# Kernel tuning notes

Hardware: AMD Instinct MI355X
Metric: run time of the kernel (lower is better)

## Reference

```python
import jax, jax.numpy as jnp
import numpy as np

N, E, F, H, G = 50000, 800000, 64, 64, 100

def setup_inputs() -> dict:
    key = jax.random.key(0)
    ks = jax.random.split(key, 12)
    x = jax.random.normal(ks[0], (N, F), dtype=jnp.float32)
    edge_index = jax.random.randint(ks[1], (2, E), 0, N, dtype=jnp.int64)
    batch = jnp.sort(jax.random.randint(ks[2], (N,), 0, G, dtype=jnp.int64))
    s1 = 1.0 / np.sqrt(F); s2 = 1.0 / np.sqrt(H)
    W1 = jax.random.normal(ks[3], (2, F, H), dtype=jnp.float32) * s1
    b1 = jnp.zeros((H,), dtype=jnp.float32)
    W2 = jax.random.normal(ks[4], (2, H, H), dtype=jnp.float32) * s2
    b2 = jnp.zeros((H,), dtype=jnp.float32)
    gamma = jnp.ones((H,), dtype=jnp.float32)
    beta = jnp.zeros((H,), dtype=jnp.float32)
    linW = jax.random.normal(ks[5], (H, 1), dtype=jnp.float32) * s2
    linb = jnp.zeros((1,), dtype=jnp.float32)
    return {"x": x, "edge_index": edge_index, "batch": batch, "W1": W1, "b1": b1,
            "W2": W2, "b2": b2, "gamma": gamma, "beta": beta, "linW": linW, "linb": linb}

def _edge_norm(row, col, n):
    # get_laplacian(sym) + lambda_max=2: Lhat off-diag weight = -d_i^{-1/2} d_j^{-1/2}, diag = 0
    deg = jax.ops.segment_sum(jnp.ones(row.shape[0], jnp.float32), row, num_segments=n)
    dis = jnp.where(deg > 0, deg ** -0.5, 0.0)
    return -dis[row] * dis[col]

def _cheb(x, row, col, w, W, b):
    # K=2: out = T0(Lhat)x @ W0 + T1(Lhat)x @ W1 + b, T1 = Lhat x via scatter-add
    Tx1 = jax.ops.segment_sum(w[:, None] * x[row], col, num_segments=x.shape[0])
    return x @ W[0] + Tx1 @ W[1] + b

def reference(x, edge_index, batch, W1, b1, W2, b2, gamma, beta, linW, linb):
    row, col = edge_index[0], edge_index[1]
    n = x.shape[0]
    w = _edge_norm(row, col, n)
    h = _cheb(x, row, col, w, W1, b1)
    # BatchNorm1d (training-mode batch stats, eps=1e-5)
    mu = jnp.mean(h, axis=0)
    var = jnp.var(h, axis=0)
    h = (h - mu) * jax.lax.rsqrt(var + 1e-5) * gamma + beta
    # LeakyReLU (default slope 0.01)
    h = jnp.where(h >= 0, h, 0.01 * h)
    h = _cheb(h, row, col, w, W2, b2)
    # global_mean_pool over graph ids
    sums = jax.ops.segment_sum(h, batch, num_segments=G)
    cnts = jax.ops.segment_sum(jnp.ones(n, jnp.float32), batch, num_segments=G)
    pooled = sums / jnp.maximum(cnts, 1.0)[:, None]
    # dropout: identity (eval)
    return pooled @ linW + linb
```

## Files before the change

### kernel.cpp

```cpp
#include <hip/hip_runtime.h>

#define HDIM 64
#define BH 64
#define HNODES 25600
#define HBINS 12800
#define SBINS 12544
#define GR 32


__device__ __forceinline__ int lbound(const int* __restrict__ b, int n, int v) {
    int lo = 0, hi = n;
    while (lo < hi) { int m = (lo + hi) >> 1; if (b[m] < v) lo = m + 1; else hi = m; }
    return lo;
}


__global__ __launch_bounds__(256) void k_histP(const int* __restrict__ row,
                                               const int* __restrict__ col,
                                               unsigned short* __restrict__ cntP,
                                               unsigned short* __restrict__ degP,
                                               int E, int N, int slice) {
    __shared__ unsigned hbin[HBINS];
    int blk   = blockIdx.x;
    int phase = blockIdx.y & 1;
    int isRow = blockIdx.y >> 1;
    const int* keys = isRow ? row : col;
    unsigned short* outP = isRow ? degP : cntP;
    int lo = phase * HNODES;
    int spanN = min(HNODES, N - lo);
    int binsU = (spanN + 1) >> 1;
    for (int i = threadIdx.x; i < binsU; i += 256) hbin[i] = 0;
    __syncthreads();
    int e0 = blk * slice, e1 = min(e0 + slice, E);
    for (int e = e0 + threadIdx.x; e < e1; e += 256) {
        int c = keys[e] - lo;
        if ((unsigned)c < (unsigned)spanN)
            atomicAdd(&hbin[c >> 1], 1u << ((c & 1) << 4));
    }
    __syncthreads();
    unsigned* outU = (unsigned*)(outP + (size_t)blk * N + lo);
    for (int i = threadIdx.x; i < binsU; i += 256) outU[i] = hbin[i];
}

__global__ void k_prefA(unsigned short* __restrict__ cntP,
                        const unsigned short* __restrict__ degP,
                        int* __restrict__ cnt, float* __restrict__ dis, int N) {
    int i = blockIdx.x * blockDim.x + threadIdx.x;
    if (i >= N) return;
    int run = 0;
    #pragma unroll 8
    for (int b = 0; b < BH; ++b) {
        int v = cntP[(size_t)b * N + i];
        cntP[(size_t)b * N + i] = (unsigned short)run;
        run += v;
    }
    cnt[i] = run;
    int d = 0;
    #pragma unroll 8
    for (int b = 0; b < BH; ++b) d += degP[(size_t)b * N + i];
    dis[i] = d > 0 ? rsqrtf((float)d) : 0.0f;
}

__global__ __launch_bounds__(1024) void k_scan1(const int* __restrict__ cnt,
                                                int* __restrict__ start,
                                                int* __restrict__ bsum, int n) {
    __shared__ int wsum[16];
    int i = blockIdx.x * 1024 + threadIdx.x;
    int lane = threadIdx.x & 63, w = threadIdx.x >> 6;
    int v = (i < n) ? cnt[i] : 0;
    int incl = v;
    #pragma unroll
    for (int off = 1; off < 64; off <<= 1) {
        int u = __shfl_up(incl, off, 64);
        if (lane >= off) incl += u;
    }
    if (lane == 63) wsum[w] = incl;
    __syncthreads();
    if (w == 0) {
        int s = (lane < 16) ? wsum[lane] : 0;
        int si = s;
        #pragma unroll
        for (int off = 1; off < 16; off <<= 1) {
            int u = __shfl_up(si, off, 64);
            if (lane >= off) si += u;
        }
        if (lane < 16) wsum[lane] = si - s;
    }
    __syncthreads();
    int excl = incl - v + wsum[w];
    if (i < n) start[i] = excl;
    if (threadIdx.x == 1023) bsum[blockIdx.x] = excl + v;
}

__global__ void k_scan2(int* __restrict__ bsum, int nb) {
    int lane = threadIdx.x;
    if (lane >= 64) return;
    int v = (lane < nb) ? bsum[lane] : 0;
    int incl = v;
    #pragma unroll
    for (int off = 1; off < 64; off <<= 1) {
        int u = __shfl_up(incl, off, 64);
        if (lane >= off) incl += u;
    }
    if (lane < nb) bsum[lane] = incl - v;
}

__global__ void k_scan3(int* __restrict__ start, const int* __restrict__ bsum, int n) {
    int i = blockIdx.x * blockDim.x + threadIdx.x;
    if (i < n) start[i] += bsum[i >> 10];
}

__global__ __launch_bounds__(256) void k_sortfill(const int* __restrict__ row,
                                                  const int* __restrict__ col,
                                                  const unsigned short* __restrict__ cntP,
                                                  const int* __restrict__ start,
                                                  int* __restrict__ er,
                                                  int E, int N, int slice) {
    __shared__ int cur[SBINS];
    int blk = blockIdx.x;
    int lo = blockIdx.y * SBINS;
    int span = min(SBINS, N - lo);
    for (int i = threadIdx.x; i < span; i += 256)
        cur[i] = start[lo + i] + (int)cntP[(size_t)blk * N + lo + i];
    __syncthreads();
    int e0 = blk * slice, e1 = min(e0 + slice, E);
    for (int e = e0 + threadIdx.x; e < e1; e += 256) {
        int c = col[e] - lo;
        int rv = row[e];
        if ((unsigned)c < (unsigned)span) {
            int pos = atomicAdd(&cur[c], 1);
            er[pos] = rv;
        }
    }
}


__global__ __launch_bounds__(256) void k_gather1(const int* __restrict__ er,
                                                 const int* __restrict__ start,
                                                 const int* __restrict__ cnt,
                                                 const float* __restrict__ dis,
                                                 const float* __restrict__ x,
                                                 float* __restrict__ Tx, int n) {
    int i = blockIdx.x * 4 + (threadIdx.x >> 6);
    if (i >= n) return;
    int lane = threadIdx.x & 63;
    int q = lane >> 4;
    int s4 = (lane & 15) * 4;
    int s = start[i], nd = cnt[i];
    float di = dis[i];
    float4 acc = make_float4(0.f, 0.f, 0.f, 0.f);
    int k = q;
    for (; k + 4 < nd; k += 8) {
        int r0 = er[s + k], r1 = er[s + k + 4];
        float w0 = -dis[r0] * di, w1 = -dis[r1] * di;
        float4 v0 = *reinterpret_cast<const float4*>(&x[(size_t)r0 * HDIM + s4]);
        float4 v1 = *reinterpret_cast<const float4*>(&x[(size_t)r1 * HDIM + s4]);
        acc.x = fmaf(w0, v0.x, acc.x); acc.y = fmaf(w0, v0.y, acc.y);
        acc.z = fmaf(w0, v0.z, acc.z); acc.w = fmaf(w0, v0.w, acc.w);
        acc.x = fmaf(w1, v1.x, acc.x); acc.y = fmaf(w1, v1.y, acc.y);
        acc.z = fmaf(w1, v1.z, acc.z); acc.w = fmaf(w1, v1.w, acc.w);
    }
    if (k < nd) {
        int r0 = er[s + k];
        float w0 = -dis[r0] * di;
        float4 v0 = *reinterpret_cast<const float4*>(&x[(size_t)r0 * HDIM + s4]);
        acc.x = fmaf(w0, v0.x, acc.x); acc.y = fmaf(w0, v0.y, acc.y);
        acc.z = fmaf(w0, v0.z, acc.z); acc.w = fmaf(w0, v0.w, acc.w);
    }
    #pragma unroll
    for (int off = 16; off <= 32; off <<= 1) {
        acc.x += __shfl_xor(acc.x, off, 64);
        acc.y += __shfl_xor(acc.y, off, 64);
        acc.z += __shfl_xor(acc.z, off, 64);
        acc.w += __shfl_xor(acc.w, off, 64);
    }
    if (q == 0) *reinterpret_cast<float4*>(&Tx[(size_t)i * HDIM + s4]) = acc;
}

__global__ __launch_bounds__(256) void k_gemm1(const float* __restrict__ x,
                                               float* __restrict__ TxH,
                                               const float* __restrict__ W1,
                                               const float* __restrict__ b1,
                                               float* __restrict__ stats, int n) {
    __shared__ float xs[GR][HDIM];
    __shared__ float ts[GR][HDIM];
    int tid = threadIdx.x;
    int j = tid & 63, w = tid >> 6;

    float4 w0r[16], w1r[16];
    #pragma unroll
    for (int k4 = 0; k4 < 16; ++k4) {
        w0r[k4].x = W1[(k4 * 4 + 0) * HDIM + j];
        w0r[k4].y = W1[(k4 * 4 + 1) * HDIM + j];
        w0r[k4].z = W1[(k4 * 4 + 2) * HDIM + j];
        w0r[k4].w = W1[(k4 * 4 + 3) * HDIM + j];
        w1r[k4].x = W1[4096 + (k4 * 4 + 0) * HDIM + j];
        w1r[k4].y = W1[4096 + (k4 * 4 + 1) * HDIM + j];
        w1r[k4].z = W1[4096 + (k4 * 4 + 2) * HDIM + j];
        w1r[k4].w = W1[4096 + (k4 * 4 + 3) * HDIM + j];
    }
    float bj = b1[j];
    float sacc = 0.f, ssacc = 0.f;

    for (int base = blockIdx.x * GR; base < n; base += gridDim.x * GR) {
        __syncthreads();
        for (int v = tid; v < GR * HDIM / 4; v += 256) {
            int r = base + (v >> 4);
            if (r < n) {
                int c = (v & 15) * 4;
                ((float4*)xs)[v] = *(const float4*)&x[(size_t)r * HDIM + c];
                ((float4*)ts)[v] = *(const float4*)&TxH[(size_t)r * HDIM + c];
            }
        }
        __syncthreads();
        #pragma unroll
        for (int m = 0; m < 8; ++m) {
            int lr = w * 8 + m;
            int r = base + lr;
            if (r < n) {
                const float4* xr = (const float4*)xs[lr];
                const float4* tr = (const float4*)ts[lr];
                float acc = bj;
                #pragma unroll
                for (int k4 = 0; k4 < 16; ++k4) {
                    float4 xv = xr[k4], tv = tr[k4];
                    acc = fmaf(xv.x, w0r[k4].x, acc);
                    acc = fmaf(xv.y, w0r[k4].y, acc);
                    acc = fmaf(xv.z, w0r[k4].z, acc);
                    acc = fmaf(xv.w, w0r[k4].w, acc);
                    acc = fmaf(tv.x, w1r[k4].x, acc);
                    acc = fmaf(tv.y, w1r[k4].y, acc);
                    acc = fmaf(tv.z, w1r[k4].z, acc);
                    acc = fmaf(tv.w, w1r[k4].w, acc);
                }
                TxH[(size_t)r * HDIM + j] = acc;
                sacc += acc;
                ssacc = fmaf(acc, acc, ssacc);
            }
        }
    }
    __syncthreads();
    xs[w][j] = sacc;
    ts[w][j] = ssacc;
    __syncthreads();
    if (w == 0) {
        float s  = xs[0][j] + xs[1][j] + xs[2][j] + xs[3][j];
        float ss = ts[0][j] + ts[1][j] + ts[2][j] + ts[3][j];
        atomicAdd(&stats[j], s);
        atomicAdd(&stats[64 + j], ss);
    }
}

__global__ void k_prep(const float* __restrict__ stats,
                       const float* __restrict__ gamma, const float* __restrict__ beta,
                       const float* __restrict__ W2, const float* __restrict__ b2,
                       const float* __restrict__ linW, const float* __restrict__ linb,
                       float* __restrict__ scale, float* __restrict__ shift,
                       float* __restrict__ u0, float* __restrict__ u1,
                       float* __restrict__ c0, int n) {
    int k = threadIdx.x;
    if (k >= HDIM) return;
    float inv_n = 1.0f / (float)n;
    float mu  = stats[k] * inv_n;
    float var = stats[64 + k] * inv_n - mu * mu;
    float rs  = rsqrtf(var + 1e-5f);
    float sc  = rs * gamma[k];
    scale[k] = sc;
    shift[k] = beta[k] - mu * sc;
    float a0 = 0.f, a1 = 0.f;
    #pragma unroll 8
    for (int j = 0; j < HDIM; ++j) {
        float lw = linW[j];
        a0 = fmaf(W2[k * HDIM + j], lw, a0);
        a1 = fmaf(W2[HDIM * HDIM + k * HDIM + j], lw, a1);
    }
    u0[k] = a0;
    u1[k] = a1;
    if (k == 0) {
        float c = linb[0];
        for (int j = 0; j < HDIM; ++j) c = fmaf(b2[j], linW[j], c);
        c0[0] = c;
    }
}

__global__ __launch_bounds__(256) void k_node(const float* __restrict__ h,
                                              const float* __restrict__ scale,
                                              const float* __restrict__ shift,
                                              const float* __restrict__ u0,
                                              const float* __restrict__ u1,
                                              float* __restrict__ a, float* __restrict__ t,
                                              int n) {
    int i = blockIdx.x * 4 + (threadIdx.x >> 6);
    if (i >= n) return;
    int j = threadIdx.x & 63;
    float v = fmaf(h[(size_t)i * HDIM + j], scale[j], shift[j]);
    v = v >= 0.f ? v : 0.01f * v;
    float p0 = v * u0[j];
    float p1 = v * u1[j];
    #pragma unroll
    for (int off = 32; off > 0; off >>= 1) {
        p0 += __shfl_xor(p0, off, 64);
        p1 += __shfl_xor(p1, off, 64);
    }
    if (j == 0) { a[i] = p0; t[i] = p1; }
}

__global__ void k_gather2(const int* __restrict__ er, const int* __restrict__ start,
                          const int* __restrict__ cnt, const float* __restrict__ dis,
                          const float* __restrict__ t, const float* __restrict__ a,
                          float* __restrict__ s2, int n) {
    int i = blockIdx.x * blockDim.x + threadIdx.x;
    if (i >= n) return;
    int s = start[i], nd = cnt[i];
    float di = dis[i];
    float acc = a[i];
    int k = 0;
    for (; k + 1 < nd; k += 2) {
        int r0 = er[s + k], r1 = er[s + k + 1];
        float v0 = -dis[r0] * di * t[r0];
        float v1 = -dis[r1] * di * t[r1];
        acc += v0 + v1;
    }
    if (k < nd) {
        int r0 = er[s + k];
        acc = fmaf(-dis[r0] * di, t[r0], acc);
    }
    s2[i] = acc;
}

__global__ __launch_bounds__(256) void k_pool2(const float* __restrict__ s2,
                                               const int* __restrict__ batch,
                                               const float* __restrict__ c0,
                                               const float* __restrict__ linb,
                                               float* __restrict__ out, int n) {
    int g = blockIdx.x;
    int lo = lbound(batch, n, g);
    int hi = lbound(batch, n, g + 1);
    float s = 0.f;
    for (int i = lo + threadIdx.x; i < hi; i += 256) s += s2[i];
    __shared__ float red[256];
    red[threadIdx.x] = s;
    __syncthreads();
    for (int off = 128; off > 0; off >>= 1) {
        if (threadIdx.x < off) red[threadIdx.x] += red[threadIdx.x + off];
        __syncthreads();
    }
    if (threadIdx.x == 0) {
        int cntg = hi - lo;
        out[g] = cntg > 0 ? red[0] / (float)cntg + c0[0] : linb[0];
    }
}


extern "C" void kernel_launch(void* const* d_in, const int* in_sizes, int n_in,
                              void* d_out, int out_size, void* d_ws, size_t ws_size,
                              hipStream_t stream) {
    const float* x     = (const float*)d_in[0];
    const int*   eidx  = (const int*)d_in[1];
    const int*   batch = (const int*)d_in[2];
    const float* W1    = (const float*)d_in[3];
    const float* b1    = (const float*)d_in[4];
    const float* W2    = (const float*)d_in[5];
    const float* b2    = (const float*)d_in[6];
    const float* gamma = (const float*)d_in[7];
    const float* beta  = (const float*)d_in[8];
    const float* linW  = (const float*)d_in[9];
    const float* linb  = (const float*)d_in[10];
    float* out = (float*)d_out;

    const int N = in_sizes[0] / HDIM;
    const int E = in_sizes[1] / 2;
    const int G = out_size;
    const int NB = (N + 1023) / 1024;
    const int slice = (E + BH - 1) / BH;

    const int* row = eidx;
    const int* col = eidx + E;

    char* wsb = (char*)d_ws;
    float* TxH  = (float*)wsb;               wsb += (size_t)N * HDIM * 4;
    unsigned short* cntP = (unsigned short*)TxH;
    unsigned short* degP = cntP + (size_t)BH * N;
    int*   cnt   = (int*)wsb;                wsb += (size_t)N * 4;
    int*   start = (int*)wsb;                wsb += (size_t)N * 4;
    int*   bsum  = (int*)wsb;                wsb += (size_t)NB * 4 + 64;
    int*   er    = (int*)wsb;                wsb += (size_t)E * 4;
    float* dis   = (float*)wsb;              wsb += (size_t)N * 4;
    float* a     = (float*)wsb;              wsb += (size_t)N * 4;
    float* t     = (float*)wsb;              wsb += (size_t)N * 4;
    float* s2    = (float*)wsb;              wsb += (size_t)N * 4;
    float* stats = (float*)wsb;              wsb += 128 * 4;
    float* scale = (float*)wsb;              wsb += HDIM * 4;
    float* shift = (float*)wsb;              wsb += HDIM * 4;
    float* u0    = (float*)wsb;              wsb += HDIM * 4;
    float* u1    = (float*)wsb;              wsb += HDIM * 4;
    float* c0    = (float*)wsb;              wsb += 64;

    hipMemsetAsync(stats, 0, 128 * 4, stream);

    k_histP<<<dim3(BH, 4), 256, 0, stream>>>(row, col, cntP, degP, E, N, slice);
    k_prefA<<<(N + 255) / 256, 256, 0, stream>>>(cntP, degP, cnt, dis, N);
    k_scan1<<<NB, 1024, 0, stream>>>(cnt, start, bsum, N);
    k_scan2<<<1, 64, 0, stream>>>(bsum, NB);
    k_scan3<<<(N + 255) / 256, 256, 0, stream>>>(start, bsum, N);
    k_sortfill<<<dim3(BH, 4), 256, 0, stream>>>(row, col, cntP, start, er, E, N, slice);
    k_gather1<<<(N + 3) / 4, 256, 0, stream>>>(er, start, cnt, dis, x, TxH, N);
    k_gemm1<<<512, 256, 0, stream>>>(x, TxH, W1, b1, stats, N);
    k_prep<<<1, 64, 0, stream>>>(stats, gamma, beta, W2, b2, linW, linb,
                                 scale, shift, u0, u1, c0, N);
    k_node<<<(N + 3) / 4, 256, 0, stream>>>(TxH, scale, shift, u0, u1, a, t, N);
    k_gather2<<<(N + 255) / 256, 256, 0, stream>>>(er, start, cnt, dis, t, a, s2, N);
    k_pool2<<<G, 256, 0, stream>>>(s2, batch, c0, linb, out, N);
}
```

Baseline: 190.7 us.

## Split gemm1 K dimension across thread halves and replace stat atomics with two-stage reduction

The first-layer GEMM kernel now runs one 512-thread block per 32-row tile. One half of the threads multiplies x by W0 and the other half multiplies Tx by W1, and the partial sums are combined through shared memory. This halves the per-thread weight registers and raises parallelism in place of a persistent grid-stride loop. The BatchNorm sum and sum-of-squares statistics are written as per-block partials and reduced by a new kernel, which removes the global atomics and the memset. The cost is an extra kernel launch, a partial-stat buffer, and more blocks each reloading W1.

After: 169.0 us. 11.4% less time.

```diff
diff --git a/kernel.cpp b/kernel.cpp
--- a/kernel.cpp
+++ b/kernel.cpp
@@ -177,78 +177,107 @@
     if (q == 0) *reinterpret_cast<float4*>(&Tx[(size_t)i * HDIM + s4]) = acc;
 }
 
-__global__ __launch_bounds__(256) void k_gemm1(const float* __restrict__ x,
+__global__ __launch_bounds__(512) void k_gemm1(const float* __restrict__ x,
                                                float* __restrict__ TxH,
                                                const float* __restrict__ W1,
                                                const float* __restrict__ b1,
-                                               float* __restrict__ stats, int n) {
+                                               float* __restrict__ pstat, int n) {
     __shared__ float xs[GR][HDIM];
     __shared__ float ts[GR][HDIM];
-    int tid = threadIdx.x;
-    int j = tid & 63, w = tid >> 6;
-
-    float4 w0r[16], w1r[16];
+    __shared__ float pl[GR][HDIM];
+    int tid  = threadIdx.x;
+    int j    = tid & 63;
+    int half = (tid >> 6) & 1;
+    int w2   = tid >> 7;
+    int base = blockIdx.x * GR;
+
+    const float* Wb = W1 + (half ? HDIM * HDIM : 0);
+    float4 wr[16];
     #pragma unroll
     for (int k4 = 0; k4 < 16; ++k4) {
-        w0r[k4].x = W1[(k4 * 4 + 0) * HDIM + j];
-        w0r[k4].y = W1[(k4 * 4 + 1) * HDIM + j];
-        w0r[k4].z = W1[(k4 * 4 + 2) * HDIM + j];
-        w0r[k4].w = W1[(k4 * 4 + 3) * HDIM + j];
-        w1r[k4].x = W1[4096 + (k4 * 4 + 0) * HDIM + j];
-        w1r[k4].y = W1[4096 + (k4 * 4 + 1) * HDIM + j];
-        w1r[k4].z = W1[4096 + (k4 * 4 + 2) * HDIM + j];
-        w1r[k4].w = W1[4096 + (k4 * 4 + 3) * HDIM + j];
+        wr[k4].x = Wb[(k4 * 4 + 0) * HDIM + j];
+        wr[k4].y = Wb[(k4 * 4 + 1) * HDIM + j];
+        wr[k4].z = Wb[(k4 * 4 + 2) * HDIM + j];
+        wr[k4].w = Wb[(k4 * 4 + 3) * HDIM + j];
     }
     float bj = b1[j];
+
+    {
+        int v = tid;
+        int r = base + (v >> 4);
+        int rc = min(r, n - 1);
+        int c = (v & 15) * 4;
+        ((float4*)xs)[v] = *(const float4*)&x[(size_t)rc * HDIM + c];
+        ((float4*)ts)[v] = *(const float4*)&TxH[(size_t)rc * HDIM + c];
+    }
+    __syncthreads();
+
+    const float(*src)[HDIM] = half ? ts : xs;
+    float acc[8];
+    #pragma unroll
+    for (int m = 0; m < 8; ++m) {
+        int lr = w2 * 8 + m;
+        const float4* rp = (const float4*)src[lr];
+        float a = 0.f;
+        #pragma unroll
+        for (int k4 = 0; k4 < 16; ++k4) {
+            float4 v = rp[k4];
+            a = fmaf(v.x, wr[k4].x, a);
+            a = fmaf(v.y, wr[k4].y, a);
+            a = fmaf(v.z, wr[k4].z, a);
+            a = fmaf(v.w, wr[k4].w, a);
+        }
+        acc[m] = a;
+    }
+
+    if (half == 1) {
+        #pragma unroll
+        for (int m = 0; m < 8; ++m) pl[w2 * 8 + m][j] = acc[m];
+    }
+    __syncthreads();
+
     float sacc = 0.f, ssacc = 0.f;
-
-    for (int base = blockIdx.x * GR; base < n; base += gridDim.x * GR) {
-        __syncthreads();
-        for (int v = tid; v < GR * HDIM / 4; v += 256) {
-            int r = base + (v >> 4);
+    if (half == 0) {
+        #pragma unroll
+        for (int m = 0; m < 8; ++m) {
+            int lr = w2 * 8 + m;
+            int r = base + lr;
             if (r < n) {
-                int c = (v & 15) * 4;
-                ((float4*)xs)[v] = *(const float4*)&x[(size_t)r * HDIM + c];
-                ((float4*)ts)[v] = *(const float4*)&TxH[(size_t)r * HDIM + c];
+                float tot = acc[m] + pl[lr][j] + bj;
+                TxH[(size_t)r * HDIM + j] = tot;
+                sacc += tot;
+                ssacc = fmaf(tot, tot, ssacc);
             }
         }
+    }
+    __syncthreads();
+    if (half == 0) {
+        pl[w2][j]     = sacc;
+        pl[4 + w2][j] = ssacc;
+    }
+    __syncthreads();
+    if (half == 0 && w2 == 0) {
+        float s  = pl[0][j] + pl[1][j] + pl[2][j] + pl[3][j];
+        float ss = pl[4][j] + pl[5][j] + pl[6][j] + pl[7][j];
+        pstat[(size_t)blockIdx.x * 128 + j]      = s;
+        pstat[(size_t)blockIdx.x * 128 + 64 + j] = ss;
+    }
+}
+
+__global__ __launch_bounds__(256) void k_statred(const float* __restrict__ pstat,
+                                                 float* __restrict__ stats, int nb) {
+    int idx = blockIdx.x;
+    float s = 0.f;
+    for (int b = threadIdx.x; b < nb; b += 256)
+        s += pstat[(size_t)b * 128 + idx];
+    __shared__ float red[256];
+    red[threadIdx.x] = s;
+    __syncthreads();
+    for (int off = 128; off > 0; off >>= 1) {
+        if (threadIdx.x < off) red[threadIdx.x] += red[threadIdx.x + off];
         __syncthreads();
-        #pragma unroll
-        for (int m = 0; m < 8; ++m) {
-            int lr = w * 8 + m;
-            int r = base + lr;
-            if (r < n) {
-                const float4* xr = (const float4*)xs[lr];
-                const float4* tr = (const float4*)ts[lr];
-                float acc = bj;
-                #pragma unroll
-                for (int k4 = 0; k4 < 16; ++k4) {
-                    float4 xv = xr[k4], tv = tr[k4];
-                    acc = fmaf(xv.x, w0r[k4].x, acc);
-                    acc = fmaf(xv.y, w0r[k4].y, acc);
-                    acc = fmaf(xv.z, w0r[k4].z, acc);
-                    acc = fmaf(xv.w, w0r[k4].w, acc);
-                    acc = fmaf(tv.x, w1r[k4].x, acc);
-                    acc = fmaf(tv.y, w1r[k4].y, acc);
-                    acc = fmaf(tv.z, w1r[k4].z, acc);
-                    acc = fmaf(tv.w, w1r[k4].w, acc);
-                }
-                TxH[(size_t)r * HDIM + j] = acc;
-                sacc += acc;
-                ssacc = fmaf(acc, acc, ssacc);
-            }
-        }
-    }
-    __syncthreads();
-    xs[w][j] = sacc;
-    ts[w][j] = ssacc;
-    __syncthreads();
-    if (w == 0) {
-        float s  = xs[0][j] + xs[1][j] + xs[2][j] + xs[3][j];
-        float ss = ts[0][j] + ts[1][j] + ts[2][j] + ts[3][j];
-        atomicAdd(&stats[j], s);
-        atomicAdd(&stats[64 + j], ss);
-    }
+    }
+    if (threadIdx.x == 0) stats[idx] = red[0];
 }
 
 __global__ void k_prep(const float* __restrict__ stats,
@@ -373,6 +402,7 @@
     const int G = out_size;
     const int NB = (N + 1023) / 1024;
     const int slice = (E + BH - 1) / BH;
+    const int NGB = (N + GR - 1) / GR;
 
     const int* row = eidx;
     const int* col = eidx + E;
@@ -389,14 +419,13 @@
     float* a     = (float*)wsb;              wsb += (size_t)N * 4;
     float* t     = (float*)wsb;              wsb += (size_t)N * 4;
     float* s2    = (float*)wsb;              wsb += (size_t)N * 4;
+    float* pstat = (float*)wsb;              wsb += (size_t)NGB * 128 * 4;
     float* stats = (float*)wsb;              wsb += 128 * 4;
     float* scale = (float*)wsb;              wsb += HDIM * 4;
     float* shift = (float*)wsb;              wsb += HDIM * 4;
     float* u0    = (float*)wsb;              wsb += HDIM * 4;
     float* u1    = (float*)wsb;              wsb += HDIM * 4;
     float* c0    = (float*)wsb;              wsb += 64;
-
-    hipMemsetAsync(stats, 0, 128 * 4, stream);
 
     k_histP<<<dim3(BH, 4), 256, 0, stream>>>(row, col, cntP, degP, E, N, slice);
     k_prefA<<<(N + 255) / 256, 256, 0, stream>>>(cntP, degP, cnt, dis, N);
@@ -405,7 +434,8 @@
     k_scan3<<<(N + 255) / 256, 256, 0, stream>>>(start, bsum, N);
     k_sortfill<<<dim3(BH, 4), 256, 0, stream>>>(row, col, cntP, start, er, E, N, slice);
     k_gather1<<<(N + 3) / 4, 256, 0, stream>>>(er, start, cnt, dis, x, TxH, N);
-    k_gemm1<<<512, 256, 0, stream>>>(x, TxH, W1, b1, stats, N);
+    k_gemm1<<<NGB, 512, 0, stream>>>(x, TxH, W1, b1, pstat, N);
+    k_statred<<<128, 256, 0, stream>>>(pstat, stats, NGB);
     k_prep<<<1, 64, 0, stream>>>(stats, gamma, beta, W2, b2, linW, linb,
                                  scale, shift, u0, u1, c0, N);
     k_node<<<(N + 3) / 4, 256, 0, stream>>>(TxH, scale, shift, u0, u1, a, t, N);
```
